# Kernel tuning notes

Hardware: AMD Instinct MI355X
Metric: run time of the kernel (lower is better)

Reference implementation:

```python
import jax, jax.numpy as jnp
import numpy as np

B, S, HALF = 8, 2048, 512
D = 2 * HALF  # input_dim

def setup_inputs() -> dict:
    key = jax.random.key(0)
    ks = jax.random.split(key, 8)
    scale = 1.0 / np.sqrt(D)
    return {
        "t_out": jax.random.normal(ks[0], (B, S, HALF), dtype=jnp.float32),
        "c_out": jax.random.normal(ks[1], (B, S, HALF), dtype=jnp.float32),
        "Wq": jax.random.uniform(ks[2], (D, D), jnp.float32, -scale, scale),
        "bq": jax.random.uniform(ks[3], (D,), jnp.float32, -scale, scale),
        "Wk": jax.random.uniform(ks[4], (D, D), jnp.float32, -scale, scale),
        "bk": jax.random.uniform(ks[5], (D,), jnp.float32, -scale, scale),
        "Wv": jax.random.uniform(ks[6], (D, D), jnp.float32, -scale, scale),
        "bv": jax.random.uniform(ks[7], (D,), jnp.float32, -scale, scale),
    }

def reference(t_out, c_out, Wq, bq, Wk, bk, Wv, bv):
    # combined: [B, S, D]
    combined = jnp.concatenate([t_out, c_out], axis=-1)
    # torch nn.Linear: y = x @ W.T + b
    q = jnp.einsum('bsd,ed->bse', combined, Wq) + bq
    k = jnp.einsum('bsd,ed->bse', combined, Wk) + bk
    v = jnp.einsum('bsd,ed->bse', combined, Wv) + bv
    # Unscaled dot-product attention (no 1/sqrt(d) factor in original)
    scores = jnp.einsum('bqd,bkd->bqk', q, k)  # [B, S, S]
    attn = jax.nn.softmax(scores, axis=-1)
    return jnp.einsum('bqk,bkd->bqd', attn, v)
```

## Files before the change

kernel.cpp:

```cpp
#include <hip/hip_runtime.h>
#include <cstdint>
#include <cstddef>

typedef _Float16 f16;
typedef __attribute__((ext_vector_type(4))) _Float16 f16x4;
typedef __attribute__((ext_vector_type(8))) _Float16 f16x8;
typedef __attribute__((ext_vector_type(4))) float f32x4;

#define MFMA_F16(a, b, c) __builtin_amdgcn_mfma_f32_16x16x32_f16((a), (b), (c), 0, 0, 0)

static constexpr int BB   = 8;
static constexpr int SS   = 2048;
static constexpr int DD   = 1024;
static constexpr int HALF = 512;
static constexpr int T32  = 256 * 32;

__device__ __forceinline__ void gll16(const f16* g, f16* lds) {
  __builtin_amdgcn_global_load_lds(
      (__attribute__((address_space(1))) void*)(g),
      (__attribute__((address_space(3))) void*)(lds), 16, 0, 0);
}

__device__ __forceinline__ dim3 xcd_swz() {
  const int gx = gridDim.x, gy = gridDim.y;
  const int lin = blockIdx.x + gx * (blockIdx.y + gy * blockIdx.z);
  const int nwg = gx * gy * (int)gridDim.z;
  const int q = nwg >> 3;
  const int nlin = (lin & 7) * q + (lin >> 3);
  dim3 r;
  r.x = nlin % gx;
  const int rest = nlin / gx;
  r.y = rest % gy;
  r.z = rest / gy;
  return r;
}

__global__ __launch_bounds__(256) void fused_prep(
    const float* __restrict__ Wq, const float* __restrict__ Wk, const float* __restrict__ Wv,
    const float* __restrict__ t_out, const float* __restrict__ c_out,
    f16* __restrict__ Whq, f16* __restrict__ Whk, f16* __restrict__ Whv,
    f16* __restrict__ Xh)
{
  if (blockIdx.x < 1024) {
    const int i = (blockIdx.x * 256 + threadIdx.x) * 4;
    const float4 q = *(const float4*)(Wq + i);
    const float4 k = *(const float4*)(Wk + i);
    const float4 v = *(const float4*)(Wv + i);
    f16x4 a;
    a.x = (f16)q.x; a.y = (f16)q.y; a.z = (f16)q.z; a.w = (f16)q.w; *(f16x4*)(Whq + i) = a;
    a.x = (f16)k.x; a.y = (f16)k.y; a.z = (f16)k.z; a.w = (f16)k.w; *(f16x4*)(Whk + i) = a;
    a.x = (f16)v.x; a.y = (f16)v.y; a.z = (f16)v.z; a.w = (f16)v.w; *(f16x4*)(Whv + i) = a;
  } else {
    const size_t i = ((size_t)(blockIdx.x - 1024) * 256 + threadIdx.x) * 4;
    const int d = (int)(i & 1023);
    const size_t g = i >> 10;
    const float* src = (d < HALF) ? (t_out + g * HALF + d)
                                  : (c_out + g * HALF + (d - HALF));
    const float4 x = *(const float4*)src;
    f16x4 h;
    h.x = (f16)x.x; h.y = (f16)x.y; h.z = (f16)x.z; h.w = (f16)x.w;
    *(f16x4*)(Xh + i) = h;
  }
}

__device__ __forceinline__ void stage_half(
    f16* s, const f16* g, size_t r0, int ld, int k0, int u, int w4, int rr, int gg)
{
#pragma unroll
  for (int q = 0; q < 2; ++q) {
    const int rb  = u * 128 + w4 * 32 + q * 16;
    const int row = rb + rr;
    const int lg  = gg ^ ((row >> 1) & 3);
    gll16(g + (r0 + (size_t)row) * ld + k0 + lg * 8, s + (size_t)rb * 32);
  }
}

template <int K>
__device__ __forceinline__ void mma_pipeline(
    const f16* __restrict__ A, const f16* __restrict__ B,
    int lda, int ldb, size_t arow0, size_t brow0,
    f16* As, f16* Bs, f32x4 acc[8][4],
    int wave, int lane, int wm, int wn, int col16, int quad)
{
  constexpr int NT = K / 32;
  const int w4 = wave & 3, rr = lane >> 2, gg = lane & 3;
  const f16*  g_st  = (wave < 4) ? A : B;
  const size_t r0_st = (wave < 4) ? arow0 : brow0;
  const int    ld_st = (wave < 4) ? lda : ldb;
  f16*         ring  = (wave < 4) ? As : Bs;

#pragma unroll
  for (int pt = 0; pt < 3; ++pt)
#pragma unroll
    for (int u = 0; u < 2; ++u)
      stage_half(ring + pt * T32, g_st, r0_st, ld_st, pt * 32, u, w4, rr, gg);
  asm volatile("s_waitcnt vmcnt(8)" ::: "memory");
  __builtin_amdgcn_s_barrier();

  for (int t = 0; t < NT; ++t) {
    const f16* At = As + (t & 3) * T32;
    const f16* Bt = Bs + (t & 3) * T32;
    f16* Sn = ring + ((t + 3) & 3) * T32;
    const bool st = (t + 3 < NT);
    const int kn = (t + 3) * 32;

    f16x8 a[4], b[4];

#pragma unroll
    for (int j = 0; j < 4; ++j) {
      const int r = wn * 64 + j * 16 + col16;
      b[j] = *(const f16x8*)&Bt[r * 32 + ((quad ^ ((r >> 1) & 3)) << 3)];
    }
#pragma unroll
    for (int i = 0; i < 4; ++i) {
      const int r = wm * 128 + i * 16 + col16;
      a[i] = *(const f16x8*)&At[r * 32 + ((quad ^ ((r >> 1) & 3)) << 3)];
    }
    if (st) stage_half(Sn, g_st, r0_st, ld_st, kn, 0, w4, rr, gg);
    if (t < NT - 3)       asm volatile("s_waitcnt vmcnt(6)" ::: "memory");
    else if (t == NT - 3) asm volatile("s_waitcnt vmcnt(4)" ::: "memory");
    else                  asm volatile("s_waitcnt vmcnt(0)" ::: "memory");
    __builtin_amdgcn_s_barrier();
    asm volatile("s_waitcnt lgkmcnt(0)" ::: "memory");
    __builtin_amdgcn_sched_barrier(0);
    __builtin_amdgcn_s_setprio(1);
#pragma unroll
    for (int i = 0; i < 4; ++i)
#pragma unroll
      for (int j = 0; j < 4; ++j)
        acc[i][j] = MFMA_F16(a[i], b[j], acc[i][j]);
    __builtin_amdgcn_s_setprio(0);
    __builtin_amdgcn_s_barrier();

#pragma unroll
    for (int i = 0; i < 4; ++i) {
      const int r = wm * 128 + 64 + i * 16 + col16;
      a[i] = *(const f16x8*)&At[r * 32 + ((quad ^ ((r >> 1) & 3)) << 3)];
    }
    if (st) stage_half(Sn, g_st, r0_st, ld_st, kn, 1, w4, rr, gg);
    __builtin_amdgcn_s_barrier();
    asm volatile("s_waitcnt lgkmcnt(0)" ::: "memory");
    __builtin_amdgcn_sched_barrier(0);
    __builtin_amdgcn_s_setprio(1);
#pragma unroll
    for (int i = 0; i < 4; ++i)
#pragma unroll
      for (int j = 0; j < 4; ++j)
        acc[i + 4][j] = MFMA_F16(a[i], b[j], acc[i + 4][j]);
    __builtin_amdgcn_s_setprio(0);
    __builtin_amdgcn_s_barrier();
  }
}

__global__ __launch_bounds__(512, 2) void proj_gemm(
    const f16* __restrict__ Xh,
    const f16* __restrict__ Whq, const f16* __restrict__ Whk, const f16* __restrict__ Whv,
    const float* __restrict__ bq, const float* __restrict__ bk, const float* __restrict__ bv,
    f16* __restrict__ Q, f16* __restrict__ K, f16* __restrict__ Vv)
{
  __shared__ alignas(16) f16 As[4 * T32];
  __shared__ alignas(16) f16 Bs[4 * T32];

  const int z = blockIdx.z;
  const f16* Wh = (z == 0) ? Whq : (z == 1) ? Whk : Whv;
  const float* bias = (z == 0) ? bq : (z == 1) ? bk : bv;
  f16* dst = (z == 0) ? Q : (z == 1) ? K : Vv;

  const int t = threadIdx.x, lane = t & 63, wave = t >> 6;
  const int wm = wave >> 2, wn = wave & 3, col16 = lane & 15, quad = lane >> 4;
  const int m0 = blockIdx.x * 256, n0 = blockIdx.y * 256;

  f32x4 acc[8][4];
#pragma unroll
  for (int i = 0; i < 8; ++i)
#pragma unroll
    for (int j = 0; j < 4; ++j) acc[i][j] = f32x4{0.f, 0.f, 0.f, 0.f};

  mma_pipeline<DD>(Xh, Wh, DD, DD, (size_t)m0, (size_t)n0,
                   As, Bs, acc, wave, lane, wm, wn, col16, quad);

#pragma unroll
  for (int j = 0; j < 4; ++j) {
    const int gn = n0 + wn * 64 + j * 16 + col16;
    const float bb_ = bias[gn];
#pragma unroll
    for (int i = 0; i < 8; ++i) {
      const int gm = m0 + wm * 128 + i * 16 + quad * 4;
#pragma unroll
      for (int r = 0; r < 4; ++r)
        dst[(size_t)(gm + r) * DD + gn] = (f16)(acc[i][j][r] + bb_);
    }
  }
}

__global__ __launch_bounds__(256) void transpose_v(
    const f16* __restrict__ Vv, f16* __restrict__ Vt)
{
  __shared__ alignas(16) f16 tile[64][72];
  const int b  = blockIdx.z;
  const int s0 = blockIdx.x * 64;
  const int e0 = blockIdx.y * 64;
  const int t  = threadIdx.x;
  const int r  = t >> 3;
  const int c8 = (t & 7) * 8;

  const f16* src0 = Vv + ((size_t)(b * SS + s0 + r)) * DD + e0 + c8;
  const f16* src1 = Vv + ((size_t)(b * SS + s0 + r + 32)) * DD + e0 + c8;
  *(int4*)&tile[r][c8]      = *(const int4*)src0;
  *(int4*)&tile[r + 32][c8] = *(const int4*)src1;
  __syncthreads();

  f16x8 v0, v1;
#pragma unroll
  for (int u = 0; u < 8; ++u) {
    v0[u] = tile[c8 + u][r];
    v1[u] = tile[c8 + u][r + 32];
  }
  f16* dst0 = Vt + ((size_t)b * DD + e0 + r) * SS + s0 + c8;
  f16* dst1 = Vt + ((size_t)b * DD + e0 + r + 32) * SS + s0 + c8;
  *(f16x8*)dst0 = v0;
  *(f16x8*)dst1 = v1;
}

__global__ __launch_bounds__(512, 2) void qk_gemm(
    const f16* __restrict__ Q, const f16* __restrict__ K, f16* __restrict__ Sc,
    int b0)
{
  __shared__ alignas(16) f16 As[4 * T32];
  __shared__ alignas(16) f16 Bs[4 * T32];

  const dim3 bid = xcd_swz();
  const int bb = bid.z;
  const int t = threadIdx.x, lane = t & 63, wave = t >> 6;
  const int wm = wave >> 2, wn = wave & 3, col16 = lane & 15, quad = lane >> 4;
  const int m0 = bid.y * 256, n0 = bid.x * 256;

  const size_t arow0 = (size_t)(b0 + bb) * SS + m0;
  const size_t brow0 = (size_t)(b0 + bb) * SS + n0;

  f32x4 acc[8][4];
#pragma unroll
  for (int i = 0; i < 8; ++i)
#pragma unroll
    for (int j = 0; j < 4; ++j) acc[i][j] = f32x4{0.f, 0.f, 0.f, 0.f};

  mma_pipeline<DD>(Q, K, DD, DD, arow0, brow0,
                   As, Bs, acc, wave, lane, wm, wn, col16, quad);

#pragma unroll
  for (int i = 0; i < 8; ++i)
#pragma unroll
    for (int j = 0; j < 4; ++j)
#pragma unroll
      for (int r = 0; r < 4; ++r) {
        const int gm = m0 + wm * 128 + i * 16 + quad * 4 + r;
        const int gn = n0 + wn * 64 + j * 16 + col16;
        Sc[((size_t)bb * SS + gm) * SS + gn] = (f16)acc[i][j][r];
      }
}

__global__ __launch_bounds__(256) void softmax_rows(f16* __restrict__ Sc)
{
  const size_t row = blockIdx.x;
  f16* p = Sc + row * SS;
  const int t = threadIdx.x;

  const f16x8 v = *(const f16x8*)(p + t * 8);
  float xs[8];
#pragma unroll
  for (int u = 0; u < 8; ++u) xs[u] = (float)v[u];

  float m = xs[0];
#pragma unroll
  for (int u = 1; u < 8; ++u) m = fmaxf(m, xs[u]);
#pragma unroll
  for (int off = 32; off > 0; off >>= 1) m = fmaxf(m, __shfl_xor(m, off));
  __shared__ float redm[4];
  __shared__ float reds[4];
  if ((t & 63) == 0) redm[t >> 6] = m;
  __syncthreads();
  m = fmaxf(fmaxf(redm[0], redm[1]), fmaxf(redm[2], redm[3]));

  float e[8];
  float s = 0.f;
#pragma unroll
  for (int u = 0; u < 8; ++u) {
    e[u] = expf(xs[u] - m);
    s += e[u];
  }
#pragma unroll
  for (int off = 32; off > 0; off >>= 1) s += __shfl_xor(s, off);
  if ((t & 63) == 0) reds[t >> 6] = s;
  __syncthreads();
  s = reds[0] + reds[1] + reds[2] + reds[3];
  const float inv = 1.0f / s;

  f16x8 o;
#pragma unroll
  for (int u = 0; u < 8; ++u) o[u] = (f16)(e[u] * inv);
  *(f16x8*)(p + t * 8) = o;
}

__global__ __launch_bounds__(512, 2) void pv_gemm(
    const f16* __restrict__ P, const f16* __restrict__ Vt, float* __restrict__ out,
    int b0)
{
  __shared__ alignas(16) f16 As[4 * T32];
  __shared__ alignas(16) f16 Bs[4 * T32];

  const dim3 bid = xcd_swz();
  const int bb = bid.z;
  const int t = threadIdx.x, lane = t & 63, wave = t >> 6;
  const int wm = wave >> 2, wn = wave & 3, col16 = lane & 15, quad = lane >> 4;
  const int m0 = bid.y * 256;
  const int n0 = bid.x * 256;

  const size_t arow0 = (size_t)bb * SS + m0;
  const size_t brow0 = (size_t)(b0 + bb) * DD + n0;

  f32x4 acc[8][4];
#pragma unroll
  for (int i = 0; i < 8; ++i)
#pragma unroll
    for (int j = 0; j < 4; ++j) acc[i][j] = f32x4{0.f, 0.f, 0.f, 0.f};

  mma_pipeline<SS>(P, Vt, SS, SS, arow0, brow0,
                   As, Bs, acc, wave, lane, wm, wn, col16, quad);

#pragma unroll
  for (int i = 0; i < 8; ++i)
#pragma unroll
    for (int j = 0; j < 4; ++j)
#pragma unroll
      for (int r = 0; r < 4; ++r) {
        const int gm = m0 + wm * 128 + i * 16 + quad * 4 + r;
        const int gn = n0 + wn * 64 + j * 16 + col16;
        out[((size_t)(b0 + bb) * SS + gm) * DD + gn] = acc[i][j][r];
      }
}

extern "C" void kernel_launch(void* const* d_in, const int* in_sizes, int n_in,
                              void* d_out, int out_size, void* d_ws, size_t ws_size,
                              hipStream_t stream)
{
  const float* t_out = (const float*)d_in[0];
  const float* c_out = (const float*)d_in[1];
  const float* Wq    = (const float*)d_in[2];
  const float* bq    = (const float*)d_in[3];
  const float* Wk    = (const float*)d_in[4];
  const float* bk    = (const float*)d_in[5];
  const float* Wv    = (const float*)d_in[6];
  const float* bv    = (const float*)d_in[7];
  float* out = (float*)d_out;

  const size_t WELT  = (size_t)DD * DD;
  const size_t TD8   = (size_t)BB * SS * DD;
  const size_t XH_B  = TD8 * sizeof(f16);
  const size_t SC1_B = (size_t)SS * SS * sizeof(f16);

  const size_t FIXED = 3 * WELT * sizeof(f16) + 4 * XH_B;
  int c = 2;
  for (int cand : {8, 4}) {
    size_t xsc = (size_t)cand * SC1_B;
    if (xsc < XH_B) xsc = XH_B;
    if (FIXED + xsc <= ws_size) { c = cand; break; }
  }
  size_t xsc_bytes = (size_t)c * SC1_B;
  if (xsc_bytes < XH_B) xsc_bytes = XH_B;

  char* ws = (char*)d_ws;
  f16* Whq = (f16*)ws;
  f16* Whk = Whq + WELT;
  f16* Whv = Whk + WELT;
  char* XSc = (char*)(Whv + WELT);
  f16* Xh = (f16*)XSc;
  f16* Sc = (f16*)XSc;
  f16* Q  = (f16*)(XSc + xsc_bytes);
  f16* K  = Q  + TD8;
  f16* Vv = K  + TD8;
  f16* Vt = Vv + TD8;

  fused_prep<<<dim3(1024 + 16384), dim3(256), 0, stream>>>(
      Wq, Wk, Wv, t_out, c_out, Whq, Whk, Whv, Xh);
  proj_gemm<<<dim3(64, 4, 3), dim3(512), 0, stream>>>(
      Xh, Whq, Whk, Whv, bq, bk, bv, Q, K, Vv);
  transpose_v<<<dim3(32, 16, 8), dim3(256), 0, stream>>>(Vv, Vt);

  for (int b0 = 0; b0 < BB; b0 += c) {
    qk_gemm<<<dim3(8, 8, c), dim3(512), 0, stream>>>(Q, K, Sc, b0);
    softmax_rows<<<dim3(c * SS), dim3(256), 0, stream>>>(Sc);
    pv_gemm<<<dim3(4, 8, c), dim3(512), 0, stream>>>(Sc, Vt, out, b0);
  }
}
```

Baseline: 430.8 us.

## Switch GEMMs to 32x32 MFMA with fragment prefetch, fuse V transpose, single batch launch

```diff
diff --git a/kernel.cpp b/kernel.cpp
--- a/kernel.cpp
+++ b/kernel.cpp
@@ -5,9 +5,9 @@
 typedef _Float16 f16;
 typedef __attribute__((ext_vector_type(4))) _Float16 f16x4;
 typedef __attribute__((ext_vector_type(8))) _Float16 f16x8;
-typedef __attribute__((ext_vector_type(4))) float f32x4;
-
-#define MFMA_F16(a, b, c) __builtin_amdgcn_mfma_f32_16x16x32_f16((a), (b), (c), 0, 0, 0)
+typedef __attribute__((ext_vector_type(16))) float f32x16;
+
+#define MFMA32(a, b, c) __builtin_amdgcn_mfma_f32_32x32x16_f16((a), (b), (c), 0, 0, 0)
 
 static constexpr int BB   = 8;
 static constexpr int SS   = 2048;
@@ -75,15 +75,73 @@
   }
 }
 
+__device__ __forceinline__ f16x8 rdfrag(const f16* tile, int row, int lg) {
+  const int phys = lg ^ ((row >> 1) & 3);
+  return *(const f16x8*)&tile[row * 32 + phys * 8];
+}
+
+template <bool STAGE, int VM, bool NEXT>
+__device__ __forceinline__ void tile32(
+    int t, const f16* As, const f16* Bs, f16* ring,
+    const f16* g_st, size_t r0_st, int ld_st,
+    f32x16 (&acc)[4][2], f16x8 (&a0)[4], f16x8 (&b0)[2],
+    int w4, int rr, int gg, int wm, int wn, int ln31, int kg)
+{
+  const f16* At = As + (t & 3) * T32;
+  const f16* Bt = Bs + (t & 3) * T32;
+
+  f16x8 a1[4], b1[2];
+#pragma unroll
+  for (int i = 0; i < 4; ++i) a1[i] = rdfrag(At, wm * 128 + i * 32 + ln31, 2 + kg);
+#pragma unroll
+  for (int j = 0; j < 2; ++j) b1[j] = rdfrag(Bt, wn * 64 + j * 32 + ln31, 2 + kg);
+
+  if constexpr (VM == 4) asm volatile("s_waitcnt vmcnt(4)" ::: "memory");
+  if constexpr (VM == 0) asm volatile("s_waitcnt vmcnt(0)" ::: "memory");
+  __builtin_amdgcn_s_barrier();
+  __builtin_amdgcn_sched_barrier(0);
+
+  f16* Sn = ring + ((t + 3) & 3) * T32;
+  const int kn = (t + 3) * 32;
+  if constexpr (STAGE) stage_half(Sn, g_st, r0_st, ld_st, kn, 0, w4, rr, gg);
+
+  __builtin_amdgcn_s_setprio(1);
+#pragma unroll
+  for (int i = 0; i < 4; ++i)
+#pragma unroll
+    for (int j = 0; j < 2; ++j)
+      acc[i][j] = MFMA32(a0[i], b0[j], acc[i][j]);
+  __builtin_amdgcn_s_setprio(0);
+
+  if constexpr (NEXT) {
+    const f16* At1 = As + ((t + 1) & 3) * T32;
+    const f16* Bt1 = Bs + ((t + 1) & 3) * T32;
+#pragma unroll
+    for (int i = 0; i < 4; ++i) a0[i] = rdfrag(At1, wm * 128 + i * 32 + ln31, kg);
+#pragma unroll
+    for (int j = 0; j < 2; ++j) b0[j] = rdfrag(Bt1, wn * 64 + j * 32 + ln31, kg);
+  }
+  if constexpr (STAGE) stage_half(Sn, g_st, r0_st, ld_st, kn, 1, w4, rr, gg);
+
+  __builtin_amdgcn_s_setprio(1);
+#pragma unroll
+  for (int i = 0; i < 4; ++i)
+#pragma unroll
+    for (int j = 0; j < 2; ++j)
+      acc[i][j] = MFMA32(a1[i], b1[j], acc[i][j]);
+  __builtin_amdgcn_s_setprio(0);
+}
+
 template <int K>
-__device__ __forceinline__ void mma_pipeline(
+__device__ __forceinline__ void mma_pipeline32(
     const f16* __restrict__ A, const f16* __restrict__ B,
     int lda, int ldb, size_t arow0, size_t brow0,
-    f16* As, f16* Bs, f32x4 acc[8][4],
-    int wave, int lane, int wm, int wn, int col16, int quad)
+    f16* As, f16* Bs, f32x16 (&acc)[4][2],
+    int wave, int lane, int wm, int wn)
 {
   constexpr int NT = K / 32;
   const int w4 = wave & 3, rr = lane >> 2, gg = lane & 3;
+  const int ln31 = lane & 31, kg = lane >> 5;
   const f16*  g_st  = (wave < 4) ? A : B;
   const size_t r0_st = (wave < 4) ? arow0 : brow0;
   const int    ld_st = (wave < 4) ? lda : ldb;
@@ -97,166 +155,144 @@
   asm volatile("s_waitcnt vmcnt(8)" ::: "memory");
   __builtin_amdgcn_s_barrier();
 
-  for (int t = 0; t < NT; ++t) {
-    const f16* At = As + (t & 3) * T32;
-    const f16* Bt = Bs + (t & 3) * T32;
-    f16* Sn = ring + ((t + 3) & 3) * T32;
-    const bool st = (t + 3 < NT);
-    const int kn = (t + 3) * 32;
-
-    f16x8 a[4], b[4];
-
-#pragma unroll
-    for (int j = 0; j < 4; ++j) {
-      const int r = wn * 64 + j * 16 + col16;
-      b[j] = *(const f16x8*)&Bt[r * 32 + ((quad ^ ((r >> 1) & 3)) << 3)];
-    }
-#pragma unroll
-    for (int i = 0; i < 4; ++i) {
-      const int r = wm * 128 + i * 16 + col16;
-      a[i] = *(const f16x8*)&At[r * 32 + ((quad ^ ((r >> 1) & 3)) << 3)];
-    }
-    if (st) stage_half(Sn, g_st, r0_st, ld_st, kn, 0, w4, rr, gg);
-    if (t < NT - 3)       asm volatile("s_waitcnt vmcnt(6)" ::: "memory");
-    else if (t == NT - 3) asm volatile("s_waitcnt vmcnt(4)" ::: "memory");
-    else                  asm volatile("s_waitcnt vmcnt(0)" ::: "memory");
-    __builtin_amdgcn_s_barrier();
-    asm volatile("s_waitcnt lgkmcnt(0)" ::: "memory");
-    __builtin_amdgcn_sched_barrier(0);
-    __builtin_amdgcn_s_setprio(1);
-#pragma unroll
-    for (int i = 0; i < 4; ++i)
-#pragma unroll
-      for (int j = 0; j < 4; ++j)
-        acc[i][j] = MFMA_F16(a[i], b[j], acc[i][j]);
-    __builtin_amdgcn_s_setprio(0);
-    __builtin_amdgcn_s_barrier();
-
-#pragma unroll
-    for (int i = 0; i < 4; ++i) {
-      const int r = wm * 128 + 64 + i * 16 + col16;
-      a[i] = *(const f16x8*)&At[r * 32 + ((quad ^ ((r >> 1) & 3)) << 3)];
-    }
-    if (st) stage_half(Sn, g_st, r0_st, ld_st, kn, 1, w4, rr, gg);
-    __builtin_amdgcn_s_barrier();
-    asm volatile("s_waitcnt lgkmcnt(0)" ::: "memory");
-    __builtin_amdgcn_sched_barrier(0);
-    __builtin_amdgcn_s_setprio(1);
-#pragma unroll
-    for (int i = 0; i < 4; ++i)
-#pragma unroll
-      for (int j = 0; j < 4; ++j)
-        acc[i + 4][j] = MFMA_F16(a[i], b[j], acc[i + 4][j]);
-    __builtin_amdgcn_s_setprio(0);
-    __builtin_amdgcn_s_barrier();
-  }
+  f16x8 a0[4], b0[2];
+#pragma unroll
+  for (int i = 0; i < 4; ++i) a0[i] = rdfrag(As, wm * 128 + i * 32 + ln31, kg);
+#pragma unroll
+  for (int j = 0; j < 2; ++j) b0[j] = rdfrag(Bs, wn * 64 + j * 32 + ln31, kg);
+
+  for (int t = 0; t < NT - 3; ++t)
+    tile32<true, 4, true>(t, As, Bs, ring, g_st, r0_st, ld_st, acc, a0, b0,
+                          w4, rr, gg, wm, wn, ln31, kg);
+  tile32<false, 4, true>(NT - 3, As, Bs, ring, g_st, r0_st, ld_st, acc, a0, b0,
+                         w4, rr, gg, wm, wn, ln31, kg);
+  tile32<false, 0, true>(NT - 2, As, Bs, ring, g_st, r0_st, ld_st, acc, a0, b0,
+                         w4, rr, gg, wm, wn, ln31, kg);
+  tile32<false, -1, false>(NT - 1, As, Bs, ring, g_st, r0_st, ld_st, acc, a0, b0,
+                           w4, rr, gg, wm, wn, ln31, kg);
 }
 
 __global__ __launch_bounds__(512, 2) void proj_gemm(
     const f16* __restrict__ Xh,
     const f16* __restrict__ Whq, const f16* __restrict__ Whk, const f16* __restrict__ Whv,
     const float* __restrict__ bq, const float* __restrict__ bk, const float* __restrict__ bv,
-    f16* __restrict__ Q, f16* __restrict__ K, f16* __restrict__ Vv)
-{
-  __shared__ alignas(16) f16 As[4 * T32];
-  __shared__ alignas(16) f16 Bs[4 * T32];
+    f16* __restrict__ Q, f16* __restrict__ K, f16* __restrict__ Vt)
+{
+  __shared__ alignas(16) f16 SMEM[8 * T32];
+  f16* As = SMEM;
+  f16* Bs = SMEM + 4 * T32;
 
   const int z = blockIdx.z;
   const f16* Wh = (z == 0) ? Whq : (z == 1) ? Whk : Whv;
   const float* bias = (z == 0) ? bq : (z == 1) ? bk : bv;
-  f16* dst = (z == 0) ? Q : (z == 1) ? K : Vv;
 
   const int t = threadIdx.x, lane = t & 63, wave = t >> 6;
-  const int wm = wave >> 2, wn = wave & 3, col16 = lane & 15, quad = lane >> 4;
+  const int wm = wave >> 2, wn = wave & 3;
+  const int ln31 = lane & 31, kg = lane >> 5;
   const int m0 = blockIdx.x * 256, n0 = blockIdx.y * 256;
 
-  f32x4 acc[8][4];
-#pragma unroll
-  for (int i = 0; i < 8; ++i)
-#pragma unroll
-    for (int j = 0; j < 4; ++j) acc[i][j] = f32x4{0.f, 0.f, 0.f, 0.f};
-
-  mma_pipeline<DD>(Xh, Wh, DD, DD, (size_t)m0, (size_t)n0,
-                   As, Bs, acc, wave, lane, wm, wn, col16, quad);
-
-#pragma unroll
-  for (int j = 0; j < 4; ++j) {
-    const int gn = n0 + wn * 64 + j * 16 + col16;
-    const float bb_ = bias[gn];
-#pragma unroll
-    for (int i = 0; i < 8; ++i) {
-      const int gm = m0 + wm * 128 + i * 16 + quad * 4;
-#pragma unroll
-      for (int r = 0; r < 4; ++r)
-        dst[(size_t)(gm + r) * DD + gn] = (f16)(acc[i][j][r] + bb_);
+  f32x16 acc[4][2];
+#pragma unroll
+  for (int i = 0; i < 4; ++i)
+#pragma unroll
+    for (int j = 0; j < 2; ++j)
+#pragma unroll
+      for (int r = 0; r < 16; ++r) acc[i][j][r] = 0.f;
+
+  mma_pipeline32<DD>(Xh, Wh, DD, DD, (size_t)m0, (size_t)n0,
+                     As, Bs, acc, wave, lane, wm, wn);
+
+  if (z < 2) {
+    f16* dst = (z == 0) ? Q : K;
+#pragma unroll
+    for (int j = 0; j < 2; ++j) {
+      const int gn = n0 + wn * 64 + j * 32 + ln31;
+      const float bb_ = bias[gn];
+#pragma unroll
+      for (int i = 0; i < 4; ++i)
+#pragma unroll
+        for (int r = 0; r < 16; ++r) {
+          const int gm = m0 + wm * 128 + i * 32 + (r & 3) + 8 * (r >> 2) + 4 * kg;
+          dst[(size_t)gm * DD + gn] = (f16)(acc[i][j][r] + bb_);
+        }
     }
-  }
-}
-
-__global__ __launch_bounds__(256) void transpose_v(
-    const f16* __restrict__ Vv, f16* __restrict__ Vt)
-{
-  __shared__ alignas(16) f16 tile[64][72];
-  const int b  = blockIdx.z;
-  const int s0 = blockIdx.x * 64;
-  const int e0 = blockIdx.y * 64;
-  const int t  = threadIdx.x;
-  const int r  = t >> 3;
-  const int c8 = (t & 7) * 8;
-
-  const f16* src0 = Vv + ((size_t)(b * SS + s0 + r)) * DD + e0 + c8;
-  const f16* src1 = Vv + ((size_t)(b * SS + s0 + r + 32)) * DD + e0 + c8;
-  *(int4*)&tile[r][c8]      = *(const int4*)src0;
-  *(int4*)&tile[r + 32][c8] = *(const int4*)src1;
-  __syncthreads();
-
-  f16x8 v0, v1;
-#pragma unroll
-  for (int u = 0; u < 8; ++u) {
-    v0[u] = tile[c8 + u][r];
-    v1[u] = tile[c8 + u][r + 32];
-  }
-  f16* dst0 = Vt + ((size_t)b * DD + e0 + r) * SS + s0 + c8;
-  f16* dst1 = Vt + ((size_t)b * DD + e0 + r + 32) * SS + s0 + c8;
-  *(f16x8*)dst0 = v0;
-  *(f16x8*)dst1 = v1;
+  } else {
+    __syncthreads();
+    constexpr int RL = 136;
+    f16* tb = SMEM;
+    const int bV = m0 >> 11;
+    const int s0 = m0 & 2047;
+    for (int h = 0; h < 2; ++h) {
+      if (wm == h) {
+#pragma unroll
+        for (int j = 0; j < 2; ++j) {
+          const int e = wn * 64 + j * 32 + ln31;
+          const float bb_ = bias[n0 + e];
+#pragma unroll
+          for (int i = 0; i < 4; ++i)
+#pragma unroll
+            for (int g2 = 0; g2 < 4; ++g2) {
+              const int m = i * 32 + g2 * 8 + 4 * kg;
+              f16x4 pk;
+              pk.x = (f16)(acc[i][j][g2 * 4 + 0] + bb_);
+              pk.y = (f16)(acc[i][j][g2 * 4 + 1] + bb_);
+              pk.z = (f16)(acc[i][j][g2 * 4 + 2] + bb_);
+              pk.w = (f16)(acc[i][j][g2 * 4 + 3] + bb_);
+              *(f16x4*)&tb[e * RL + m] = pk;
+            }
+        }
+      }
+      __syncthreads();
+#pragma unroll
+      for (int p = 0; p < 8; ++p) {
+        const int idx = p * 512 + t;
+        const int e = idx >> 4, mc = idx & 15;
+        const f16x8 v = *(const f16x8*)&tb[e * RL + mc * 8];
+        *(f16x8*)&Vt[((size_t)bV * DD + n0 + e) * SS + s0 + h * 128 + mc * 8] = v;
+      }
+      __syncthreads();
+    }
+  }
 }
 
 __global__ __launch_bounds__(512, 2) void qk_gemm(
-    const f16* __restrict__ Q, const f16* __restrict__ K, f16* __restrict__ Sc,
-    int b0)
-{
-  __shared__ alignas(16) f16 As[4 * T32];
-  __shared__ alignas(16) f16 Bs[4 * T32];
+    const f16* __restrict__ Q, const f16* __restrict__ K, f16* __restrict__ Sc)
+{
+  __shared__ alignas(16) f16 SMEM[8 * T32];
+  f16* As = SMEM;
+  f16* Bs = SMEM + 4 * T32;
 
   const dim3 bid = xcd_swz();
   const int bb = bid.z;
   const int t = threadIdx.x, lane = t & 63, wave = t >> 6;
-  const int wm = wave >> 2, wn = wave & 3, col16 = lane & 15, quad = lane >> 4;
+  const int wm = wave >> 2, wn = wave & 3;
+  const int ln31 = lane & 31, kg = lane >> 5;
   const int m0 = bid.y * 256, n0 = bid.x * 256;
 
-  const size_t arow0 = (size_t)(b0 + bb) * SS + m0;
-  const size_t brow0 = (size_t)(b0 + bb) * SS + n0;
-
-  f32x4 acc[8][4];
-#pragma unroll
-  for (int i = 0; i < 8; ++i)
-#pragma unroll
-    for (int j = 0; j < 4; ++j) acc[i][j] = f32x4{0.f, 0.f, 0.f, 0.f};
-
-  mma_pipeline<DD>(Q, K, DD, DD, arow0, brow0,
-                   As, Bs, acc, wave, lane, wm, wn, col16, quad);
-
-#pragma unroll
-  for (int i = 0; i < 8; ++i)
-#pragma unroll
-    for (int j = 0; j < 4; ++j)
-#pragma unroll
-      for (int r = 0; r < 4; ++r) {
-        const int gm = m0 + wm * 128 + i * 16 + quad * 4 + r;
-        const int gn = n0 + wn * 64 + j * 16 + col16;
+  const size_t arow0 = (size_t)bb * SS + m0;
+  const size_t brow0 = (size_t)bb * SS + n0;
+
+  f32x16 acc[4][2];
+#pragma unroll
+  for (int i = 0; i < 4; ++i)
+#pragma unroll
+    for (int j = 0; j < 2; ++j)
+#pragma unroll
+      for (int r = 0; r < 16; ++r) acc[i][j][r] = 0.f;
+
+  mma_pipeline32<DD>(Q, K, DD, DD, arow0, brow0, As, Bs, acc, wave, lane, wm, wn);
+
+#pragma unroll
+  for (int j = 0; j < 2; ++j) {
+    const int gn = n0 + wn * 64 + j * 32 + ln31;
+#pragma unroll
+    for (int i = 0; i < 4; ++i)
+#pragma unroll
+      for (int r = 0; r < 16; ++r) {
+        const int gm = m0 + wm * 128 + i * 32 + (r & 3) + 8 * (r >> 2) + 4 * kg;
         Sc[((size_t)bb * SS + gm) * SS + gn] = (f16)acc[i][j][r];
       }
+  }
 }
 
 __global__ __launch_bounds__(256) void softmax_rows(f16* __restrict__ Sc)
@@ -302,41 +338,44 @@
 }
 
 __global__ __launch_bounds__(512, 2) void pv_gemm(
-    const f16* __restrict__ P, const f16* __restrict__ Vt, float* __restrict__ out,
-    int b0)
-{
-  __shared__ alignas(16) f16 As[4 * T32];
-  __shared__ alignas(16) f16 Bs[4 * T32];
+    const f16* __restrict__ P, const f16* __restrict__ Vt, float* __restrict__ out)
+{
+  __shared__ alignas(16) f16 SMEM[8 * T32];
+  f16* As = SMEM;
+  f16* Bs = SMEM + 4 * T32;
 
   const dim3 bid = xcd_swz();
   const int bb = bid.z;
   const int t = threadIdx.x, lane = t & 63, wave = t >> 6;
-  const int wm = wave >> 2, wn = wave & 3, col16 = lane & 15, quad = lane >> 4;
+  const int wm = wave >> 2, wn = wave & 3;
+  const int ln31 = lane & 31, kg = lane >> 5;
   const int m0 = bid.y * 256;
   const int n0 = bid.x * 256;
 
   const size_t arow0 = (size_t)bb * SS + m0;
-  const size_t brow0 = (size_t)(b0 + bb) * DD + n0;
-
-  f32x4 acc[8][4];
-#pragma unroll
-  for (int i = 0; i < 8; ++i)
-#pragma unroll
-    for (int j = 0; j < 4; ++j) acc[i][j] = f32x4{0.f, 0.f, 0.f, 0.f};
-
-  mma_pipeline<SS>(P, Vt, SS, SS, arow0, brow0,
-                   As, Bs, acc, wave, lane, wm, wn, col16, quad);
-
-#pragma unroll
-  for (int i = 0; i < 8; ++i)
-#pragma unroll
-    for (int j = 0; j < 4; ++j)
-#pragma unroll
-      for (int r = 0; r < 4; ++r) {
-        const int gm = m0 + wm * 128 + i * 16 + quad * 4 + r;
-        const int gn = n0 + wn * 64 + j * 16 + col16;
-        out[((size_t)(b0 + bb) * SS + gm) * DD + gn] = acc[i][j][r];
+  const size_t brow0 = (size_t)bb * DD + n0;
+
+  f32x16 acc[4][2];
+#pragma unroll
+  for (int i = 0; i < 4; ++i)
+#pragma unroll
+    for (int j = 0; j < 2; ++j)
+#pragma unroll
+      for (int r = 0; r < 16; ++r) acc[i][j][r] = 0.f;
+
+  mma_pipeline32<SS>(P, Vt, SS, SS, arow0, brow0, As, Bs, acc, wave, lane, wm, wn);
+
+#pragma unroll
+  for (int j = 0; j < 2; ++j) {
+    const int gn = n0 + wn * 64 + j * 32 + ln31;
+#pragma unroll
+    for (int i = 0; i < 4; ++i)
+#pragma unroll
+      for (int r = 0; r < 16; ++r) {
+        const int gm = m0 + wm * 128 + i * 32 + (r & 3) + 8 * (r >> 2) + 4 * kg;
+        out[((size_t)bb * SS + gm) * DD + gn] = acc[i][j][r];
       }
+  }
 }
 
 extern "C" void kernel_launch(void* const* d_in, const int* in_sizes, int n_in,
@@ -353,42 +392,25 @@
   const float* bv    = (const float*)d_in[7];
   float* out = (float*)d_out;
 
-  const size_t WELT  = (size_t)DD * DD;
-  const size_t TD8   = (size_t)BB * SS * DD;
-  const size_t XH_B  = TD8 * sizeof(f16);
-  const size_t SC1_B = (size_t)SS * SS * sizeof(f16);
-
-  const size_t FIXED = 3 * WELT * sizeof(f16) + 4 * XH_B;
-  int c = 2;
-  for (int cand : {8, 4}) {
-    size_t xsc = (size_t)cand * SC1_B;
-    if (xsc < XH_B) xsc = XH_B;
-    if (FIXED + xsc <= ws_size) { c = cand; break; }
-  }
-  size_t xsc_bytes = (size_t)c * SC1_B;
-  if (xsc_bytes < XH_B) xsc_bytes = XH_B;
+  const size_t WELT = (size_t)DD * DD;
+  const size_t TD8  = (size_t)BB * SS * DD;
+  const size_t SCE  = (size_t)BB * SS * SS;
 
   char* ws = (char*)d_ws;
   f16* Whq = (f16*)ws;
   f16* Whk = Whq + WELT;
   f16* Whv = Whk + WELT;
-  char* XSc = (char*)(Whv + WELT);
-  f16* Xh = (f16*)XSc;
-  f16* Sc = (f16*)XSc;
-  f16* Q  = (f16*)(XSc + xsc_bytes);
-  f16* K  = Q  + TD8;
-  f16* Vv = K  + TD8;
-  f16* Vt = Vv + TD8;
+  f16* Xh  = Whv + WELT;
+  f16* Sc  = Xh;
+  f16* Q   = Xh + SCE;
+  f16* K   = Q + TD8;
+  f16* Vt  = K + TD8;
 
   fused_prep<<<dim3(1024 + 16384), dim3(256), 0, stream>>>(
       Wq, Wk, Wv, t_out, c_out, Whq, Whk, Whv, Xh);
   proj_gemm<<<dim3(64, 4, 3), dim3(512), 0, stream>>>(
-      Xh, Whq, Whk, Whv, bq, bk, bv, Q, K, Vv);
-  transpose_v<<<dim3(32, 16, 8), dim3(256), 0, stream>>>(Vv, Vt);
-
-  for (int b0 = 0; b0 < BB; b0 += c) {
-    qk_gemm<<<dim3(8, 8, c), dim3(512), 0, stream>>>(Q, K, Sc, b0);
-    softmax_rows<<<dim3(c * SS), dim3(256), 0, stream>>>(Sc);
-    pv_gemm<<<dim3(4, 8, c), dim3(512), 0, stream>>>(Sc, Vt, out, b0);
-  }
-}
+      Xh, Whq, Whk, Whv, bq, bk, bv, Q, K, Vt);
+  qk_gemm<<<dim3(8, 8, 8), dim3(512), 0, stream>>>(Q, K, Sc);
+  softmax_rows<<<dim3(BB * SS), dim3(256), 0, stream>>>(Sc);
+  pv_gemm<<<dim3(4, 8, 8), dim3(512), 0, stream>>>(Sc, Vt, out);
+}
```

New measurement: 395.0 us. -8.3%, faster.
